# Performance work log

Measured on AMD Instinct MI355X. Metric: run time of the kernel, lower is better.

Reference implementation:

```python
import jax, jax.numpy as jnp
import numpy as np

B0, K, H, W = 8, 1, 512, 512
S, CS, NMS, M = 25, 51, 5, 2048
REG_W, COV_POW = 1.0, 0.5

def _gauss_kernel(n):
    x = jnp.linspace(-1.0, 1.0, n)
    g = jnp.exp(-x * x / 0.5)
    return g / g.sum()

def _conv1d2d(x, k1d, horizontal, pad_h, pad_w):
    # x: [B,1,H,W]; replicates torch F.conv2d with the given (possibly asymmetric) padding
    kern = k1d.reshape(1, 1, 1, -1) if horizontal else k1d.reshape(1, 1, -1, 1)
    return jax.lax.conv_general_dilated(x, kern, (1, 1), [(pad_h, pad_h), (pad_w, pad_w)],
                                        dimension_numbers=("NCHW", "OIHW", "NCHW"))

def bilinear_sample(img, pts):
    # img [B,C,H,W], pts [B,N,2] (x,y in [-1,1]); grid_sample bilinear, align_corners=False, zero padding
    Bb, C, Hh, Ww = img.shape
    x = (pts[..., 0] + 1.0) * 0.5 * Ww - 0.5
    y = (pts[..., 1] + 1.0) * 0.5 * Hh - 0.5
    x0 = jnp.floor(x); y0 = jnp.floor(y)
    wx = x - x0; wy = y - y0
    x0i = x0.astype(jnp.int32); y0i = y0.astype(jnp.int32)
    flat = img.reshape(Bb, C, Hh * Ww)
    def tap(yi, xi, w):
        ok = ((yi >= 0) & (yi < Hh) & (xi >= 0) & (xi < Ww)).astype(img.dtype)
        idx = jnp.clip(yi, 0, Hh - 1) * Ww + jnp.clip(xi, 0, Ww - 1)  # [B,N]
        v = jnp.take_along_axis(flat, idx[:, None, :], axis=2)        # [B,C,N]
        return v * (w * ok)[:, None, :]
    return (tap(y0i, x0i, (1 - wy) * (1 - wx)) + tap(y0i, x0i + 1, (1 - wy) * wx)
            + tap(y0i + 1, x0i, wy * (1 - wx)) + tap(y0i + 1, x0i + 1, wy * wx))

def compute_matchability(keypoint_p, has_depth, Bt):
    G = _gauss_kernel(S)
    # NOTE: faithful to original asymmetric padding bug: pad H while convolving along W, then pad W while convolving along H
    s = _conv1d2d(keypoint_p.reshape(Bt, 1, H, W), G, True, S // 2, 0)
    s = _conv1d2d(s, G, False, 0, S // 2)
    log_p_hat = jax.nn.log_softmax(jnp.log(s.reshape(Bt, H * W) + 1e-8), axis=-1)
    sd = _conv1d2d(has_depth.reshape(Bt, 1, H, W), G, True, 0, S // 2)
    sd = _conv1d2d(sd, G, False, S // 2, 0).reshape(Bt, H * W)
    p = sd / sd.sum(-1, keepdims=True)
    return jnp.sum(jnp.where(p > 0, p * (jnp.log(jnp.maximum(p, 1e-30)) - log_p_hat), 0.0), axis=-1)

def sample_keypoints(sm):
    # sm [B,H,W]; coverage-reweighted NMS + top-k (topk=True, subpixel=False)
    wcov = jnp.exp(-jnp.square(jnp.linspace(-2.0, 2.0, CS)))
    ld = _conv1d2d(((sm + 1e-6) * 1e4)[:, None], wcov, True, 0, CS // 2)
    ld = _conv1d2d(ld, wcov, False, CS // 2, 0)[:, 0]
    sm = sm * (ld + 1e-8) ** (-COV_POW)
    p = NMS // 2
    mx = jax.lax.reduce_window(sm, -jnp.inf, jax.lax.max, (1, NMS, NMS), (1, 1, 1),
                               [(0, 0), (p, p), (p, p)])
    sm = sm * (sm == mx)
    _, inds = jax.lax.top_k(sm.reshape(-1, H * W), M)
    xs = (jnp.arange(W) + 0.5) * 2.0 / W - 1.0
    ys = (jnp.arange(H) + 0.5) * 2.0 / H - 1.0
    grid = jnp.stack(jnp.meshgrid(xs, ys, indexing="xy"), axis=-1).reshape(H * W, 2)
    return jnp.take(grid, inds, axis=0)  # [B,M,2] normalized (x,y)

def masked_log_softmax(logits, mask):
    return jax.nn.log_softmax(jnp.where(mask, logits, -1e9), axis=-1)

def _reward(d):
    return jnp.exp(-100.0 * d)

def _forward(scoremap, gt_warp_A2B, gt_warp_B2A, valid_A2B, valid_B2A, has_depth):
    sg = jax.lax.stop_gradient
    lA = scoremap[:B0].reshape(B0, K, H * W)
    lB = scoremap[B0:].reshape(B0, K, H * W)
    logits = jnp.concatenate([lA, lB], 0)                                   # [2B,K,HW]
    kp_p = jax.nn.softmax(logits.reshape(2 * B0, K * H * W), -1).reshape(2 * B0, K, H * W).sum(1)
    match_loss = compute_matchability(kp_p, sg(has_depth), 2 * B0).mean()
    # sparse branch is under torch.set_grad_enabled(False)
    kpts_A = sample_keypoints(sg(kp_p[:B0]).reshape(B0, H, W))
    kpts_B = sample_keypoints(sg(kp_p[B0:]).reshape(B0, H, W))
    kpts_A2B = bilinear_sample(sg(gt_warp_A2B[..., 2:]).transpose(0, 3, 1, 2), kpts_A).transpose(0, 2, 1)
    kpts_B2A = bilinear_sample(sg(gt_warp_B2A[..., 2:]).transpose(0, 3, 1, 2), kpts_B).transpose(0, 2, 1)
    legit_A2B = bilinear_sample(sg(valid_A2B)[:, None], kpts_A)[:, 0] > 0   # [B,M]
    legit_B2A = bilinear_sample(sg(valid_B2A)[:, None], kpts_B)[:, 0] > 0
    dA = jnp.sqrt(jnp.sum(jnp.square(kpts_A2B[:, :, None] - kpts_B[:, None]), -1) + 1e-12).min(-1)
    dB = jnp.sqrt(jnp.sum(jnp.square(kpts_B2A[:, :, None] - kpts_A[:, None]), -1) + 1e-12).min(-1)
    rA = _reward(dA); rB = _reward(dB)
    slA = bilinear_sample(lA.reshape(B0, 1, H, W), kpts_A)[:, 0]            # [B,M]
    slB = bilinear_sample(lB.reshape(B0, 1, H, W), kpts_B)[:, 0]
    lpA = masked_log_softmax(slA, legit_A2B)
    lpB = masked_log_softmax(slB, legit_B2A)
    sparse = -jnp.sum(jnp.where(legit_A2B, rA * lpA, 0.0)) - jnp.sum(jnp.where(legit_B2A, rB * lpB, 0.0))
    return sparse + REG_W * match_loss

def setup_inputs() -> dict:
    key = jax.random.key(0)
    ks = jax.random.split(key, 6)
    scoremap = jax.random.normal(ks[0], (2 * B0, K, H, W), jnp.float32)
    gt_warp_A2B = jax.random.uniform(ks[1], (B0, H, W, 4), jnp.float32, -1.0, 1.0)
    gt_warp_B2A = jax.random.uniform(ks[2], (B0, H, W, 4), jnp.float32, -1.0, 1.0)
    valid_A2B = (jax.random.uniform(ks[3], (B0, H, W)) > 0.3).astype(jnp.float32)
    valid_B2A = (jax.random.uniform(ks[4], (B0, H, W)) > 0.3).astype(jnp.float32)
    has_depth = (jax.random.uniform(ks[5], (2 * B0, H, W)) > 0.3).astype(jnp.float32)
    return dict(scoremap=scoremap, gt_warp_A2B=gt_warp_A2B, gt_warp_B2A=gt_warp_B2A,
                valid_A2B=valid_A2B, valid_B2A=valid_B2A, has_depth=has_depth)

def reference(scoremap, gt_warp_A2B, gt_warp_B2A, valid_A2B, valid_B2A, has_depth):
    return _forward(scoremap, gt_warp_A2B, gt_warp_B2A, valid_A2B, valid_B2A, has_depth)
```

## Files before the change

### kernel.cpp

```cpp
#include <hip/hip_runtime.h>

#define HH 512
#define WW 512
#define HW_ 262144
#define NIMG 16
#define MK 2048
#define CAPB 4096
#define SCAP 32768
#define SBUFN 768

static constexpr size_t OFF_B1    = 16777216;
static constexpr size_t OFF_SMALL = 50331648;
static constexpr size_t OFF_PP   = 4849664;
static constexpr size_t OFF_WXp  = 5111808;
static constexpr size_t OFF_WYp  = 5242880;
static constexpr size_t OFF_LG   = 5373952;
static constexpr size_t OFF_SL   = 5505024;
static constexpr size_t OFF_PMIN = 5636096;
static constexpr size_t OFF_HIST = 33554432;
static constexpr size_t OFF_SURV = 33554432 + 4194304;

#define CSTRIDE 32

__device__ __forceinline__ float wred64(float v) {
  for (int m = 1; m < 64; m <<= 1) v += __shfl_xor(v, m);
  return v;
}

__device__ __forceinline__ float coh_loadf(const float* p) {
  return __hip_atomic_load(p, __ATOMIC_RELAXED, __HIP_MEMORY_SCOPE_AGENT);
}

__device__ __forceinline__ void g25_wave0(float* g) {
  int t = threadIdx.x;
  if (t < 64) {
    float raw = 0.0f;
    if (t < 25) {
      float x = -1.0f + (float)t * (2.0f / 24.0f);
      raw = expf(-(x * x) / 0.5f);
    }
    float s = raw;
    for (int m = 1; m < 64; m <<= 1) s += __shfl_xor(s, m);
    if (t < 25) g[t] = raw / s;
  }
}
__device__ __forceinline__ void w51_wave0(float* wc) {
  int t = threadIdx.x;
  if (t < 51) {
    float x = -2.0f + (float)t * (4.0f / 50.0f);
    wc[t] = expf(-x * x);
  }
}

__global__ void __launch_bounds__(256)
k_pre(const float* __restrict__ x, const float* __restrict__ hd, float* A,
      float* sume, float* sumS, float* Zb) {
  __shared__ float g[25];
  __shared__ float gp[26];
  __shared__ float red[12];
  int tid = threadIdx.x;
  g25_wave0(g);
  if (tid == 0) {
    float c = 0.0f;
    gp[0] = 0.0f;
    for (int k = 0; k < 25; k++) { c += g[k]; gp[k + 1] = c; }
  }
  size_t base = (size_t)blockIdx.x * 1024;
  size_t e = base + tid * 4;
  float4 xs = *(const float4*)(x + e);
  float4 hs = *(const float4*)(hd + e);
  __syncthreads();
  int rem = (int)(e & (HW_ - 1));
  int y = rem >> 9, x0 = rem & 511;
  float wv;
  {
    int k0 = y - 499; if (k0 < 0) k0 = 0;
    int k1 = y + 12;  if (k1 > 24) k1 = 24;
    wv = gp[k1 + 1] - gp[k0];
  }
  float cwv[4], cpv[4];
#pragma unroll
  for (int q = 0; q < 4; q++) {
    int i = x0 + q;
    int lo = i - 487; if (lo < 0) lo = 0;
    int hi = i;       if (hi > 24) hi = 24;
    cwv[q] = gp[hi + 1] - gp[lo];
    int lo2 = i - 499; if (lo2 < 0) lo2 = 0;
    int hi2 = i + 12;  if (hi2 > 24) hi2 = 24;
    cpv[q] = gp[hi2 + 1] - gp[lo2];
  }
  float e0 = expf(xs.x), e1 = expf(xs.y), e2 = expf(xs.z), e3 = expf(xs.w);
  *(float4*)(A + e) = make_float4(e0, e1, e2, e3);
  float r0 = (e0 + e1) + (e2 + e3);
  float r1 = (e0 * cwv[0] + e1 * cwv[1] + e2 * cwv[2] + e3 * cwv[3]) * wv;
  float r2 = (hs.x * cpv[0] + hs.y * cpv[1] + hs.z * cpv[2] + hs.w * cpv[3]) * wv;
  r0 = wred64(r0); r1 = wred64(r1); r2 = wred64(r2);
  int wid = tid >> 6;
  if ((tid & 63) == 0) { red[wid] = r0; red[4 + wid] = r1; red[8 + wid] = r2; }
  __syncthreads();
  if (tid == 0) {
    int img = (int)(base >> 18);
    atomicAdd(&sume[img * CSTRIDE], red[0] + red[1] + red[2] + red[3]);
    atomicAdd(&sumS[img * CSTRIDE], red[4] + red[5] + red[6] + red[7]);
    atomicAdd(&Zb[img * CSTRIDE], red[8] + red[9] + red[10] + red[11]);
  }
}

__global__ void __launch_bounds__(256)
k_hconv(const float* __restrict__ A, const float* __restrict__ hd,
        const float* __restrict__ sume, float* b12) {
  __shared__ __align__(16) float ta[512];
  __shared__ __align__(16) float th[536];
  __shared__ float g[25];
  int tid = threadIdx.x;
  int blk = blockIdx.x;
  int img = blk >> 9;
  size_t rowoff = (size_t)blk * 512;
  g25_wave0(g);
  ((float2*)ta)[tid] = *(const float2*)(A + rowoff + tid * 2);
  ((float2*)(th + 12))[tid] = *(const float2*)(hd + rowoff + tid * 2);
  if (tid < 12) { th[tid] = 0.0f; th[524 + tid] = 0.0f; }
  __syncthreads();
  float inv = 1.0f / sume[img * CSTRIDE];
  int j = 2 * tid;
  float v1a = 0.0f, v1b = 0.0f;
  if (tid >= 6 && tid <= 249) {
    float w[26];
#pragma unroll
    for (int d = 0; d < 26; d++) w[d] = ta[j - 12 + d];
#pragma unroll
    for (int d = 0; d < 25; d++) {
      v1a = fmaf(g[d], w[d], v1a);
      v1b = fmaf(g[d], w[d + 1], v1b);
    }
  }
  float v2a = 0.0f, v2b = 0.0f;
  {
    float u[26];
#pragma unroll
    for (int d = 0; d < 26; d++) u[d] = th[j + d];
#pragma unroll
    for (int d = 0; d < 25; d++) {
      v2a = fmaf(g[d], u[d], v2a);
      v2b = fmaf(g[d], u[d + 1], v2b);
    }
  }
  *(float4*)(b12 + (rowoff + j) * 2) =
      make_float4(v1a * inv, v2a, v1b * inv, v2b);
}

__global__ void __launch_bounds__(256)
k_match(const float* __restrict__ b12,
        const float* __restrict__ sume, const float* sumS, const float* Zb,
        float* macc) {
  __shared__ float g[40];
  __shared__ float red4[4];
  int tid = threadIdx.x;
  g25_wave0(g);
  if (tid >= 25 && tid < 40) g[tid] = 0.0f;
  int blk = blockIdx.x;
  int img = blk >> 6;
  int ty = (blk >> 3) & 7;
  int tx = blk & 7;
  int y0 = ty * 64, x0 = tx * 64;
  const float* base12 = b12 + (size_t)img * HW_ * 2;
  float Z = Zb[img * CSTRIDE];
  float invs = 1.0f / sume[img * CSTRIDE];
  float logS = logf(sumS[img * CSTRIDE] * invs + (float)HW_ * 1e-8f);
  __syncthreads();
  int seg = tid >> 6;
  int c = tid & 63;
  int r0 = seg * 16;
  const float* colp = base12 + (size_t)(x0 + c) * 2;
  float s[16], d[16], wreg[16];
#pragma unroll
  for (int jj = 0; jj < 16; jj++) { s[jj] = 0.f; d[jj] = 0.f; wreg[jj] = 0.f; }
  int ybase = y0 + r0 - 12;
#pragma unroll
  for (int i = 0; i < 40; i++) {
    int y = ybase + i;
    float vx = 0.0f, vy = 0.0f;
    if ((unsigned)y < 512u) {
      float2 v = *(const float2*)(colp + (size_t)y * 1024);
      vx = v.x; vy = v.y;
    }
#pragma unroll
    for (int jj = 15; jj >= 1; jj--) wreg[jj] = wreg[jj - 1];
    wreg[0] = g[i];
#pragma unroll
    for (int jj = 0; jj < 16; jj++) {
      s[jj] = fmaf(wreg[jj], vx, s[jj]);
      d[jj] = fmaf(wreg[jj], vy, d[jj]);
    }
  }
  float acc = 0.0f;
#pragma unroll
  for (int jj = 0; jj < 16; jj++) {
    float p = d[jj] / Z;
    if (p > 0.0f)
      acc += p * (logf(fmaxf(p, 1e-30f)) - (logf(s[jj] + 1e-8f) - logS));
  }
  acc = wred64(acc);
  if ((tid & 63) == 0) red4[tid >> 6] = acc;
  __syncthreads();
  if (tid == 0)
    atomicAdd(macc, red4[0] + red4[1] + red4[2] + red4[3]);
}

__global__ void __launch_bounds__(256)
k_h51(const float* __restrict__ A, const float* __restrict__ sume, float* out,
      unsigned* __restrict__ hist) {
  __shared__ float wc[51];
  __shared__ __align__(16) float ta[564];
  int tid = threadIdx.x;
  int blk = blockIdx.x;
  int img = blk >> 9;
  size_t rowoff = (size_t)blk * 512;
  w51_wave0(wc);
  if (tid < 32)
    ((uint4*)hist)[(size_t)blk * 32 + tid] = make_uint4(0u, 0u, 0u, 0u);
  float s1 = 1e4f / sume[img * CSTRIDE];
  for (int i = tid; i < 562; i += 256) {
    int j = i - 25;
    ta[i] = ((unsigned)j < 512u) ? fmaf(A[rowoff + j], s1, 1e-2f) : 0.0f;
  }
  __syncthreads();
  int j = 2 * tid;
  float w[52];
#pragma unroll
  for (int d = 0; d < 52; d++) w[d] = ta[j + d];
  float va = 0.0f, vb = 0.0f;
#pragma unroll
  for (int d = 0; d < 51; d++) {
    va = fmaf(wc[d], w[d], va);
    vb = fmaf(wc[d], w[d + 1], vb);
  }
  ((float2*)out)[blk * 256 + tid] = make_float2(va, vb);
}

__global__ void __launch_bounds__(512, 6)
k_smwnms(const float* __restrict__ A, const float* __restrict__ sume,
         const float* __restrict__ b1,
         unsigned long long* surv, unsigned* scnt, unsigned* hist) {
  __shared__ float wc[53];
  __shared__ __align__(16) float tb1[119 * 68];
  __shared__ __align__(16) float tsm[68 * 68];
  __shared__ unsigned lcnt;
  __shared__ unsigned gbase;
  float* hm = tb1;
  unsigned long long* sbuf = (unsigned long long*)(tb1 + 4352);
  int tid = threadIdx.x;
  w51_wave0(wc);
  if (tid == 51 || tid == 52) wc[tid] = 0.0f;
  if (tid == 0) lcnt = 0;
  int blk = blockIdx.x;
  int img = blk >> 6;
  int ty = (blk >> 3) & 7;
  int tx = blk & 7;
  int y0 = ty * 64, x0 = tx * 64;
  const float* base = b1 + (size_t)img * HW_;
  {
    float2 vreg[8];
    int laddr[8];
#pragma unroll
    for (int k = 0; k < 8; k++) {
      int i = tid + k * 512;
      bool ok = (i < 119 * 34);
      int r = i / 34, c2 = i - r * 34;
      int y = y0 + r - 27;
      int x = x0 + c2 * 2 - 2;
      float2 v = make_float2(0.0f, 0.0f);
      if (ok && (unsigned)y < 512u && (unsigned)x < 512u)
        v = *(const float2*)(base + (size_t)y * 512 + x);
      vreg[k] = v;
      laddr[k] = ok ? (r * 68 + c2 * 2) : -1;
    }
#pragma unroll
    for (int k = 0; k < 8; k++)
      if (laddr[k] >= 0) *(float2*)(tb1 + laddr[k]) = vreg[k];
  }
  __syncthreads();
  float inv = 1.0f / sume[img * CSTRIDE];
  const float* abase = A + (size_t)img * HW_;
  if (tid < 23 * 17) {
    int rg = tid / 17, cg = tid - rg * 17;
    int r0 = rg * 3, c0 = cg * 4;
    int nr = (r0 <= 65) ? 3 : 2;
    float2 apre[3][2];
#pragma unroll
    for (int jj = 0; jj < 3; jj++) {
      int y = y0 + r0 + jj - 2;
      int xb = x0 + c0 - 2;
      apre[jj][0] = make_float2(0.f, 0.f);
      apre[jj][1] = make_float2(0.f, 0.f);
      if ((unsigned)y < 512u) {
        const float* ar = abase + (size_t)y * 512;
        if ((unsigned)xb < 512u) apre[jj][0] = *(const float2*)(ar + xb);
        if ((unsigned)(xb + 2) < 512u) apre[jj][1] = *(const float2*)(ar + xb + 2);
      }
    }
    float a0x = 0.f, a0y = 0.f, a0z = 0.f, a0w = 0.f;
    float a1x = 0.f, a1y = 0.f, a1z = 0.f, a1w = 0.f;
    float a2x = 0.f, a2y = 0.f, a2z = 0.f, a2w = 0.f;
    float w1 = 0.f, w2 = 0.f;
    const float* tp = tb1 + r0 * 68 + c0;
#pragma unroll 4
    for (int i = 0; i < 53; i++) {
      float4 v = *(const float4*)(tp + i * 68);
      float w0 = wc[i];
      a0x = fmaf(w0, v.x, a0x); a0y = fmaf(w0, v.y, a0y);
      a0z = fmaf(w0, v.z, a0z); a0w = fmaf(w0, v.w, a0w);
      a1x = fmaf(w1, v.x, a1x); a1y = fmaf(w1, v.y, a1y);
      a1z = fmaf(w1, v.z, a1z); a1w = fmaf(w1, v.w, a1w);
      a2x = fmaf(w2, v.x, a2x); a2y = fmaf(w2, v.y, a2y);
      a2z = fmaf(w2, v.z, a2z); a2w = fmaf(w2, v.w, a2w);
      w2 = w1; w1 = w0;
    }
    auto storerow = [&](int jj, float ax, float ay, float az, float aw,
                        float2 p0, float2 p1) {
      int r = r0 + jj;
      int y = y0 + r - 2;
      int xb = x0 + c0 - 2;
      float4 res = make_float4(-3.4e38f, -3.4e38f, -3.4e38f, -3.4e38f);
      if ((unsigned)y < 512u) {
        if ((unsigned)xb < 512u) {
          res.x = (p0.x * inv) / sqrtf(ax + 1e-8f);
          res.y = (p0.y * inv) / sqrtf(ay + 1e-8f);
        }
        if ((unsigned)(xb + 2) < 512u) {
          res.z = (p1.x * inv) / sqrtf(az + 1e-8f);
          res.w = (p1.y * inv) / sqrtf(aw + 1e-8f);
        }
      }
      *(float4*)(tsm + r * 68 + c0) = res;
    };
    storerow(0, a0x, a0y, a0z, a0w, apre[0][0], apre[0][1]);
    storerow(1, a1x, a1y, a1z, a1w, apre[1][0], apre[1][1]);
    if (nr == 3) storerow(2, a2x, a2y, a2z, a2w, apre[2][0], apre[2][1]);
  }
  __syncthreads();
  for (int i = tid; i < 68 * 16; i += 512) {
    int r = i >> 4, cg = i & 15;
    const float* row = tsm + r * 68 + cg * 4;
    float4 v0 = *(const float4*)(row);
    float4 v1 = *(const float4*)(row + 4);
    float p01 = fmaxf(v0.x, v0.y), p12 = fmaxf(v0.y, v0.z);
    float p23 = fmaxf(v0.z, v0.w), p34 = fmaxf(v0.w, v1.x);
    float p45 = fmaxf(v1.x, v1.y), p56 = fmaxf(v1.y, v1.z);
    float m0 = fmaxf(fmaxf(p01, p23), v1.x);
    float m1 = fmaxf(fmaxf(p12, p34), v1.y);
    float m2 = fmaxf(fmaxf(p23, p45), v1.z);
    float m3 = fmaxf(fmaxf(p34, p56), v1.w);
    *(float4*)(hm + r * 64 + cg * 4) = make_float4(m0, m1, m2, m3);
  }
  __syncthreads();
  for (int k0 = 0; k0 < 2; k0++) {
    int i = tid + k0 * 512;
    int r = i >> 4, cb = (i & 15) * 4;
    const float* tp2 = tsm + (r + 2) * 68 + cb + 2;
    float2 va = *(const float2*)(tp2);
    float2 vb = *(const float2*)(tp2 + 2);
    float4 m0 = *(const float4*)(hm + r * 64 + cb);
    float4 m1 = *(const float4*)(hm + (r + 1) * 64 + cb);
    float4 m2 = *(const float4*)(hm + (r + 2) * 64 + cb);
    float4 m3 = *(const float4*)(hm + (r + 3) * 64 + cb);
    float4 m4 = *(const float4*)(hm + (r + 4) * 64 + cb);
    float Mx = fmaxf(fmaxf(m0.x, m1.x), fmaxf(fmaxf(m2.x, m3.x), m4.x));
    float My = fmaxf(fmaxf(m0.y, m1.y), fmaxf(fmaxf(m2.y, m3.y), m4.y));
    float Mz = fmaxf(fmaxf(m0.z, m1.z), fmaxf(fmaxf(m2.z, m3.z), m4.z));
    float Mw = fmaxf(fmaxf(m0.w, m1.w), fmaxf(fmaxf(m2.w, m3.w), m4.w));
    auto keepf = [&](float vk, float Mk, int k) {
      if (vk == Mk && vk != 0.0f) {
        unsigned p = atomicAdd(&lcnt, 1u);
        unsigned bits = __float_as_uint(vk);
        unsigned idx = (unsigned)((y0 + r) * 512 + x0 + cb + k);
        if (p < SBUFN)
          sbuf[p] = ((unsigned long long)bits << 32) |
                    (unsigned long long)(idx ^ 0xFFFFFFFFu);
        atomicAdd(&hist[(size_t)img * 65536 + (bits >> 16)], 1u);
      }
    };
    keepf(va.x, Mx, 0); keepf(va.y, My, 1);
    keepf(vb.x, Mz, 2); keepf(vb.y, Mw, 3);
  }
  __syncthreads();
  unsigned total = lcnt; if (total > SBUFN) total = SBUFN;
  if (tid == 0) gbase = atomicAdd(&scnt[img * CSTRIDE], total);
  __syncthreads();
  unsigned gb = gbase;
  for (unsigned i = tid; i < total; i += 512) {
    unsigned p = gb + i;
    if (p < SCAP) surv[(size_t)img * SCAP + p] = sbuf[i];
  }
}

__global__ void __launch_bounds__(1024)
k_select(const unsigned long long* __restrict__ surv,
         const unsigned* __restrict__ scnt,
         const unsigned* __restrict__ hist,
         const float* __restrict__ scoremap,
         const float* __restrict__ gtA, const float* __restrict__ gtB,
         const float* __restrict__ vA, const float* __restrict__ vB,
         float2* pp, float* wx, float* wy, float* lg, float* sl) {
  int img = blockIdx.x;
  __shared__ unsigned long long key[CAPB];
  __shared__ unsigned selbuf[MK];
  __shared__ unsigned wsum[16];
  __shared__ unsigned wpre[16];
  __shared__ unsigned cnts[2];
  __shared__ unsigned TbS, needS;
  int t = threadIdx.x;
  if (t < 2) cnts[t] = 0;
  const unsigned* h = hist + (size_t)img * 65536;
  int b0 = 65472 - 64 * t;
  const uint4* hv = (const uint4*)(h + b0);
  unsigned s = 0;
#pragma unroll
  for (int k = 0; k < 16; k++) {
    uint4 u = hv[k];
    s += u.x + u.y + u.z + u.w;
  }
  if (b0 == 0) s += 0x00100000u - h[0];
  unsigned inc = s;
  for (int m = 1; m < 64; m <<= 1) {
    unsigned o = __shfl_up(inc, m);
    if ((t & 63) >= m) inc += o;
  }
  if ((t & 63) == 63) wsum[t >> 6] = inc;
  __syncthreads();
  if (t < 16) {
    unsigned p = 0;
    for (int k = 0; k < 16; k++) if (k < t) p += wsum[k];
    wpre[t] = p;
  }
  __syncthreads();
  unsigned pre = wpre[t >> 6] + inc - s;
  if (pre < MK && pre + s >= MK) {
    unsigned c = pre;
    for (int k = 0; k < 64; k++) {
      int bin = 65535 - (t * 64 + k);
      unsigned cnt = (bin == 0) ? 0x00100000u : h[bin];
      if (c + cnt >= MK) { TbS = (unsigned)bin; needS = MK - c; break; }
      c += cnt;
    }
  }
  __syncthreads();
  unsigned T = TbS, need = needS;
  unsigned cnt = scnt[img * CSTRIDE]; if (cnt > SCAP) cnt = SCAP;
  const unsigned long long* sv = surv + (size_t)img * SCAP;
  for (unsigned i = t; i < SCAP; i += 1024) {
    if (i < cnt) {
      unsigned long long entry = sv[i];
      unsigned bin = (unsigned)(entry >> 48);
      if (bin > T) {
        unsigned p = atomicAdd(&cnts[0], 1u);
        if (p < MK) selbuf[p] = (unsigned)(entry & 0xFFFFFFFFull) ^ 0xFFFFFFFFu;
      } else if (bin == T) {
        unsigned p = atomicAdd(&cnts[1], 1u);
        if (p < CAPB) key[p] = entry;
      }
    }
  }
  __syncthreads();
  unsigned c1 = cnts[0]; if (c1 > MK) c1 = MK;
  unsigned bn = cnts[1];
  int n = (bn < CAPB) ? (int)bn : CAPB;
  int np2 = 2;
  while (np2 < n) np2 <<= 1;
  for (int k = t; k < np2; k += 1024)
    if (k >= n) key[k] = 0ull;
  __syncthreads();
  for (int sz = 2; sz <= np2; sz <<= 1) {
    for (int st = sz >> 1; st > 0; st >>= 1) {
      for (int i = t; i < np2; i += 1024) {
        int l = i ^ st;
        if (l > i) {
          unsigned long long a = key[i], b = key[l];
          bool up = ((i & sz) == 0);
          if (up ? (a < b) : (a > b)) { key[i] = b; key[l] = a; }
        }
      }
      __syncthreads();
    }
  }
  unsigned kk = need; if (kk > MK - c1) kk = MK - c1;
  for (unsigned m = t; m < MK - c1; m += 1024) {
    unsigned v = 0u;
    if (m < kk && m < (unsigned)n)
      v = (unsigned)(key[m] & 0xFFFFFFFFull) ^ 0xFFFFFFFFu;
    selbuf[c1 + m] = v;
  }
  __syncthreads();
  int b = (img < 8) ? img : img - 8;
  const float* gt = (img < 8) ? gtA : gtB;
  const float* vv = (img < 8) ? vA : vB;
  for (int q = t; q < MK; q += 1024) {
    int tt = img * MK + q;
    unsigned idx = selbuf[q] & (HW_ - 1);
    int hh = idx >> 9, wp = idx & 511;
    pp[tt] = make_float2((wp + 0.5f) * (2.0f / 512.0f) - 1.0f,
                         (hh + 0.5f) * (2.0f / 512.0f) - 1.0f);
    size_t pix = (size_t)b * HW_ + idx;
    float2 gxy = *(const float2*)(gt + pix * 4 + 2);
    wx[tt] = gxy.x;
    wy[tt] = gxy.y;
    lg[tt] = (vv[pix] > 0.0f) ? 1.0f : 0.0f;
    sl[tt] = scoremap[(size_t)img * HW_ + idx];
  }
}

__global__ void __launch_bounds__(256)
k_mindist(const float2* __restrict__ pp,
          const float* __restrict__ wx, const float* __restrict__ wy,
          float* pmin,
          const float* __restrict__ sl, const float* __restrict__ lg,
          float* sacc, float* macc, float* out,
          unsigned* mdone, unsigned* ldone) {
  __shared__ float2 opp[512];
  __shared__ unsigned rank_s;
  __shared__ float red[1024];
  int blk = blockIdx.x;
  int img = blk >> 5;
  int qc = (blk >> 2) & 7;
  int oc = blk & 3;
  const float2* ob = pp + (size_t)(img ^ 8) * MK + oc * 512;
  for (int k = threadIdx.x; k < 512; k += 256) opp[k] = ob[k];
  __syncthreads();
  int m = img * MK + qc * 256 + threadIdx.x;
  float ax = wx[m], ay = wy[m];
  float d[8];
#pragma unroll
  for (int u = 0; u < 8; u++) d[u] = 3.4e38f;
  for (int n = 0; n < 512; n += 8) {
#pragma unroll
    for (int u = 0; u < 8; u++) {
      float2 o = opp[n + u];
      float dx = ax - o.x, dy = ay - o.y;
      d[u] = fminf(d[u], fmaf(dx, dx, dy * dy));
    }
  }
  float d2 = fminf(fminf(fminf(d[0], d[1]), fminf(d[2], d[3])),
                   fminf(fminf(d[4], d[5]), fminf(d[6], d[7])));
  pmin[oc * (NIMG * MK) + m] = d2;
  __syncthreads();
  if (threadIdx.x == 0) {
    __threadfence();
    rank_s = atomicAdd(&mdone[img * CSTRIDE], 1u);
  }
  __syncthreads();
  if (rank_s != 31) return;
  __threadfence();
  int t = threadIdx.x;
  const int ST = NIMG * MK;
  float l0s[4], l1s[4], s0s[4], s1s[4], g0s[4], g1s[4];
#pragma unroll
  for (int u = 0; u < 4; u++) {
    int t0 = t + u * 256;
    int i0 = img * MK + t0, i1 = i0 + 1024;
    float s0 = sl[i0], s1 = sl[i1];
    float g0 = lg[i0], g1 = lg[i1];
    s0s[u] = s0; s1s[u] = s1; g0s[u] = g0; g1s[u] = g1;
    float l0 = (g0 > 0.0f) ? s0 : -1e9f;
    float l1 = (g1 > 0.0f) ? s1 : -1e9f;
    l0s[u] = l0; l1s[u] = l1;
    red[t0] = fmaxf(l0, l1);
  }
  __syncthreads();
  for (int sd = 512; sd > 0; sd >>= 1) {
    for (int k = t; k < sd; k += 256) red[k] = fmaxf(red[k], red[k + sd]);
    __syncthreads();
  }
  float mx = red[0];
  __syncthreads();
#pragma unroll
  for (int u = 0; u < 4; u++) {
    int t0 = t + u * 256;
    red[t0] = expf(l0s[u] - mx) + expf(l1s[u] - mx);
  }
  __syncthreads();
  for (int sd = 512; sd > 0; sd >>= 1) {
    for (int k = t; k < sd; k += 256) red[k] += red[k + sd];
    __syncthreads();
  }
  float lse = mx + logf(red[0]);
  __syncthreads();
#pragma unroll
  for (int u = 0; u < 4; u++) {
    int t0 = t + u * 256;
    int i0 = img * MK + t0, i1 = i0 + 1024;
    float a = 0.0f;
    if (g0s[u] > 0.0f) {
      float mn = fminf(fminf(coh_loadf(&pmin[i0]), coh_loadf(&pmin[ST + i0])),
                       fminf(coh_loadf(&pmin[2 * ST + i0]), coh_loadf(&pmin[3 * ST + i0])));
      float r0 = expf(-100.0f * sqrtf(mn + 1e-12f));
      a += r0 * (s0s[u] - lse);
    }
    if (g1s[u] > 0.0f) {
      float mn = fminf(fminf(coh_loadf(&pmin[i1]), coh_loadf(&pmin[ST + i1])),
                       fminf(coh_loadf(&pmin[2 * ST + i1]), coh_loadf(&pmin[3 * ST + i1])));
      float r1 = expf(-100.0f * sqrtf(mn + 1e-12f));
      a += r1 * (s1s[u] - lse);
    }
    red[t0] = a;
  }
  __syncthreads();
  for (int sd = 512; sd > 0; sd >>= 1) {
    for (int k = t; k < sd; k += 256) red[k] += red[k + sd];
    __syncthreads();
  }
  float tot = red[0];
  if (t == 0) {
    atomicAdd(sacc, -tot);
    __threadfence();
    unsigned dnum = atomicAdd(ldone, 1u);
    if (dnum == NIMG - 1) {
      float sv = atomicAdd(sacc, 0.0f);
      float mv = atomicAdd(macc, 0.0f);
      out[0] = sv + mv * (1.0f / 16.0f);
    }
  }
}

extern "C" void kernel_launch(void* const* d_in, const int* in_sizes, int n_in,
                              void* d_out, int out_size, void* d_ws, size_t ws_size,
                              hipStream_t stream) {
  const float* scoremap = (const float*)d_in[0];
  const float* gtA = (const float*)d_in[1];
  const float* gtB = (const float*)d_in[2];
  const float* vA  = (const float*)d_in[3];
  const float* vB  = (const float*)d_in[4];
  const float* hd  = (const float*)d_in[5];

  char* ws = (char*)d_ws;
  float* A   = (float*)(ws);
  float* B12 = (float*)(ws + OFF_B1);
  float* B1p = (float*)(ws + OFF_B1);

  char* sm = ws + OFF_SMALL;
  float*    sume   = (float*)(sm + 0);
  float*    sumS   = (float*)(sm + 2048);
  float*    Zb     = (float*)(sm + 4096);
  float*    macc   = (float*)(sm + 14336);
  float*    sacc   = (float*)(sm + 14464);
  unsigned* scnt   = (unsigned*)(sm + 16384);
  unsigned* ldone  = (unsigned*)(sm + 20480);
  unsigned* mdone  = (unsigned*)(sm + 24576);

  unsigned* hist = (unsigned*)(ws + OFF_HIST);
  unsigned long long* surv = (unsigned long long*)(ws + OFF_SURV);
  float2* pp = (float2*)(ws + OFF_PP);
  float* wx = (float*)(ws + OFF_WXp);
  float* wy = (float*)(ws + OFF_WYp);
  float* lg = (float*)(ws + OFF_LG);
  float* sl = (float*)(ws + OFF_SL);
  float* pmin = (float*)(ws + OFF_PMIN);

  float* out = (float*)d_out;

  hipMemsetAsync(sm, 0, 32768, stream);

  k_pre<<<4096, 256, 0, stream>>>(scoremap, hd, A, sume, sumS, Zb);

  k_hconv<<<8192, 256, 0, stream>>>(A, hd, sume, B12);
  k_match<<<1024, 256, 0, stream>>>(B12, sume, sumS, Zb, macc);

  k_h51<<<8192, 256, 0, stream>>>(A, sume, B1p, hist);

  k_smwnms<<<1024, 512, 0, stream>>>(A, sume, B1p, surv, scnt, hist);

  k_select<<<16, 1024, 0, stream>>>(surv, scnt, hist, scoremap, gtA, gtB,
                                    vA, vB, pp, wx, wy, lg, sl);

  k_mindist<<<512, 256, 0, stream>>>(pp, wx, wy, pmin, sl, lg,
                                     sacc, macc, out, mdone, ldone);
}
```

Measured before the change: 307.1 us.

## Split top-k selection into last-block threshold, parallel collect, and sort kernels

The histogram threshold search moves into the last finishing k_smwnms block for each image, found with an atomic done-counter. The survivor scan, previously done by 16 blocks of 1024 threads, becomes a separate 2048-block kernel that uses wave-ballot atomics to fill global selected and boundary buffers. The final kernel only sorts the boundary bin and gathers outputs. This spreads the serial per-image work across many more blocks, at the cost of an extra launch and extra global traffic.

```diff
diff --git a/kernel.cpp b/kernel.cpp
--- a/kernel.cpp
+++ b/kernel.cpp
@@ -11,6 +11,8 @@
 
 static constexpr size_t OFF_B1    = 16777216;
 static constexpr size_t OFF_SMALL = 50331648;
+static constexpr size_t OFF_SEL  = 4194304;
+static constexpr size_t OFF_BND  = 4325376;
 static constexpr size_t OFF_PP   = 4849664;
 static constexpr size_t OFF_WXp  = 5111808;
 static constexpr size_t OFF_WYp  = 5242880;
@@ -28,6 +30,9 @@
 }
 
 __device__ __forceinline__ float coh_loadf(const float* p) {
+  return __hip_atomic_load(p, __ATOMIC_RELAXED, __HIP_MEMORY_SCOPE_AGENT);
+}
+__device__ __forceinline__ unsigned coh_loadu(const unsigned* p) {
   return __hip_atomic_load(p, __ATOMIC_RELAXED, __HIP_MEMORY_SCOPE_AGENT);
 }
 
@@ -241,12 +246,16 @@
 __global__ void __launch_bounds__(512, 6)
 k_smwnms(const float* __restrict__ A, const float* __restrict__ sume,
          const float* __restrict__ b1,
-         unsigned long long* surv, unsigned* scnt, unsigned* hist) {
+         unsigned long long* surv, unsigned* scnt, unsigned* hist,
+         unsigned* Tb, unsigned* needb, unsigned* sdone) {
   __shared__ float wc[53];
   __shared__ __align__(16) float tb1[119 * 68];
   __shared__ __align__(16) float tsm[68 * 68];
   __shared__ unsigned lcnt;
   __shared__ unsigned gbase;
+  __shared__ unsigned rank_s;
+  __shared__ unsigned wsum8[8];
+  __shared__ unsigned wpre8[8];
   float* hm = tb1;
   unsigned long long* sbuf = (unsigned long long*)(tb1 + 4352);
   int tid = threadIdx.x;
@@ -392,83 +401,110 @@
     unsigned p = gb + i;
     if (p < SCAP) surv[(size_t)img * SCAP + p] = sbuf[i];
   }
+  __syncthreads();
+  if (tid == 0) {
+    __threadfence();
+    rank_s = atomicAdd(&sdone[img * CSTRIDE], 1u);
+  }
+  __syncthreads();
+  if (rank_s != 63) return;
+  {
+    const unsigned* h = hist + (size_t)img * 65536;
+    int t = tid;
+    int b0 = 65408 - 128 * t;
+    unsigned s = 0;
+    for (int k = 0; k < 128; k++) s += coh_loadu(h + b0 + k);
+    if (b0 == 0) s += 0x00100000u - coh_loadu(h);
+    unsigned inc = s;
+    for (int m = 1; m < 64; m <<= 1) {
+      unsigned o = __shfl_up(inc, m);
+      if ((t & 63) >= m) inc += o;
+    }
+    if ((t & 63) == 63) wsum8[t >> 6] = inc;
+    __syncthreads();
+    if (t < 8) {
+      unsigned p = 0;
+      for (int k = 0; k < 8; k++) if (k < t) p += wsum8[k];
+      wpre8[t] = p;
+    }
+    __syncthreads();
+    unsigned pre = wpre8[t >> 6] + inc - s;
+    if (pre < MK && pre + s >= MK) {
+      unsigned c = pre;
+      for (int k = 0; k < 128; k++) {
+        int bin = 65535 - (t * 128 + k);
+        unsigned cntb = (bin == 0) ? 0x00100000u : coh_loadu(h + bin);
+        if (c + cntb >= MK) {
+          Tb[img * CSTRIDE] = (unsigned)bin;
+          needb[img * CSTRIDE] = MK - c;
+          break;
+        }
+        c += cntb;
+      }
+    }
+  }
+}
+
+__global__ void k_collect(const unsigned long long* __restrict__ surv,
+                          const unsigned* __restrict__ scnt,
+                          const unsigned* __restrict__ Tb,
+                          unsigned* selcnt, unsigned* sel,
+                          unsigned* bcnt, unsigned long long* bnd) {
+  int blk = blockIdx.x;
+  int img = blk >> 7;
+  int i = (blk & 127) * 256 + threadIdx.x;
+  unsigned cnt = scnt[img * CSTRIDE]; if (cnt > SCAP) cnt = SCAP;
+  unsigned long long entry = ((unsigned)i < cnt) ? surv[(size_t)img * SCAP + i] : 0ull;
+  unsigned bits = (unsigned)(entry >> 32);
+  unsigned bin = bits >> 16;
+  unsigned T = Tb[img * CSTRIDE];
+  bool ok = (unsigned)i < cnt;
+  bool c1 = ok && (bin > T);
+  bool c2 = ok && (bin == T);
+  int lane = threadIdx.x & 63;
+  unsigned long long lowmask = (1ull << lane) - 1ull;
+
+  unsigned long long m1 = __ballot(c1);
+  if (m1) {
+    int leader = __ffsll(m1) - 1;
+    unsigned base = 0;
+    if (lane == leader) base = atomicAdd(&selcnt[img * CSTRIDE], (unsigned)__popcll(m1));
+    base = __shfl(base, leader);
+    if (c1) {
+      unsigned p = base + (unsigned)__popcll(m1 & lowmask);
+      if (p < MK) sel[img * MK + p] = (unsigned)(entry & 0xFFFFFFFFull) ^ 0xFFFFFFFFu;
+    }
+  }
+  unsigned long long m2 = __ballot(c2);
+  if (m2) {
+    int leader = __ffsll(m2) - 1;
+    unsigned base = 0;
+    if (lane == leader) base = atomicAdd(&bcnt[img * CSTRIDE], (unsigned)__popcll(m2));
+    base = __shfl(base, leader);
+    if (c2) {
+      unsigned p = base + (unsigned)__popcll(m2 & lowmask);
+      if (p < CAPB) bnd[(size_t)img * CAPB + p] = entry;
+    }
+  }
 }
 
 __global__ void __launch_bounds__(1024)
-k_select(const unsigned long long* __restrict__ surv,
-         const unsigned* __restrict__ scnt,
-         const unsigned* __restrict__ hist,
-         const float* __restrict__ scoremap,
-         const float* __restrict__ gtA, const float* __restrict__ gtB,
-         const float* __restrict__ vA, const float* __restrict__ vB,
-         float2* pp, float* wx, float* wy, float* lg, float* sl) {
+k_fsp(const unsigned long long* __restrict__ bnd, const unsigned* bcnt,
+      const unsigned* needb, const unsigned* selcnt,
+      const unsigned* __restrict__ sel,
+      const float* __restrict__ scoremap,
+      const float* __restrict__ gtA, const float* __restrict__ gtB,
+      const float* __restrict__ vA, const float* __restrict__ vB,
+      float2* pp, float* wx, float* wy, float* lg, float* sl) {
   int img = blockIdx.x;
   __shared__ unsigned long long key[CAPB];
-  __shared__ unsigned selbuf[MK];
-  __shared__ unsigned wsum[16];
-  __shared__ unsigned wpre[16];
-  __shared__ unsigned cnts[2];
-  __shared__ unsigned TbS, needS;
-  int t = threadIdx.x;
-  if (t < 2) cnts[t] = 0;
-  const unsigned* h = hist + (size_t)img * 65536;
-  int b0 = 65472 - 64 * t;
-  const uint4* hv = (const uint4*)(h + b0);
-  unsigned s = 0;
-#pragma unroll
-  for (int k = 0; k < 16; k++) {
-    uint4 u = hv[k];
-    s += u.x + u.y + u.z + u.w;
-  }
-  if (b0 == 0) s += 0x00100000u - h[0];
-  unsigned inc = s;
-  for (int m = 1; m < 64; m <<= 1) {
-    unsigned o = __shfl_up(inc, m);
-    if ((t & 63) >= m) inc += o;
-  }
-  if ((t & 63) == 63) wsum[t >> 6] = inc;
-  __syncthreads();
-  if (t < 16) {
-    unsigned p = 0;
-    for (int k = 0; k < 16; k++) if (k < t) p += wsum[k];
-    wpre[t] = p;
-  }
-  __syncthreads();
-  unsigned pre = wpre[t >> 6] + inc - s;
-  if (pre < MK && pre + s >= MK) {
-    unsigned c = pre;
-    for (int k = 0; k < 64; k++) {
-      int bin = 65535 - (t * 64 + k);
-      unsigned cnt = (bin == 0) ? 0x00100000u : h[bin];
-      if (c + cnt >= MK) { TbS = (unsigned)bin; needS = MK - c; break; }
-      c += cnt;
-    }
-  }
-  __syncthreads();
-  unsigned T = TbS, need = needS;
-  unsigned cnt = scnt[img * CSTRIDE]; if (cnt > SCAP) cnt = SCAP;
-  const unsigned long long* sv = surv + (size_t)img * SCAP;
-  for (unsigned i = t; i < SCAP; i += 1024) {
-    if (i < cnt) {
-      unsigned long long entry = sv[i];
-      unsigned bin = (unsigned)(entry >> 48);
-      if (bin > T) {
-        unsigned p = atomicAdd(&cnts[0], 1u);
-        if (p < MK) selbuf[p] = (unsigned)(entry & 0xFFFFFFFFull) ^ 0xFFFFFFFFu;
-      } else if (bin == T) {
-        unsigned p = atomicAdd(&cnts[1], 1u);
-        if (p < CAPB) key[p] = entry;
-      }
-    }
-  }
-  __syncthreads();
-  unsigned c1 = cnts[0]; if (c1 > MK) c1 = MK;
-  unsigned bn = cnts[1];
+  unsigned bn = bcnt[img * CSTRIDE];
   int n = (bn < CAPB) ? (int)bn : CAPB;
   int np2 = 2;
   while (np2 < n) np2 <<= 1;
+  int t = threadIdx.x;
   for (int k = t; k < np2; k += 1024)
-    if (k >= n) key[k] = 0ull;
+    key[k] = (k < n) ? bnd[(size_t)img * CAPB + k] : 0ull;
   __syncthreads();
   for (int sz = 2; sz <= np2; sz <<= 1) {
     for (int st = sz >> 1; st > 0; st >>= 1) {
@@ -483,20 +519,24 @@
       __syncthreads();
     }
   }
+  unsigned c1 = selcnt[img * CSTRIDE]; if (c1 > MK) c1 = MK;
+  unsigned need = needb[img * CSTRIDE];
   unsigned kk = need; if (kk > MK - c1) kk = MK - c1;
-  for (unsigned m = t; m < MK - c1; m += 1024) {
-    unsigned v = 0u;
-    if (m < kk && m < (unsigned)n)
-      v = (unsigned)(key[m] & 0xFFFFFFFFull) ^ 0xFFFFFFFFu;
-    selbuf[c1 + m] = v;
-  }
-  __syncthreads();
   int b = (img < 8) ? img : img - 8;
   const float* gt = (img < 8) ? gtA : gtB;
   const float* vv = (img < 8) ? vA : vB;
   for (int q = t; q < MK; q += 1024) {
+    unsigned v;
+    if ((unsigned)q < c1) {
+      v = sel[img * MK + q];
+    } else {
+      unsigned m = (unsigned)q - c1;
+      v = 0u;
+      if (m < kk && m < (unsigned)n)
+        v = (unsigned)(key[m] & 0xFFFFFFFFull) ^ 0xFFFFFFFFu;
+    }
     int tt = img * MK + q;
-    unsigned idx = selbuf[q] & (HW_ - 1);
+    unsigned idx = v & (HW_ - 1);
     int hh = idx >> 9, wp = idx & 511;
     pp[tt] = make_float2((wp + 0.5f) * (2.0f / 512.0f) - 1.0f,
                          (hh + 0.5f) * (2.0f / 512.0f) - 1.0f);
@@ -640,14 +680,21 @@
   float*    sume   = (float*)(sm + 0);
   float*    sumS   = (float*)(sm + 2048);
   float*    Zb     = (float*)(sm + 4096);
+  unsigned* Tb     = (unsigned*)(sm + 6144);
+  unsigned* needb  = (unsigned*)(sm + 8192);
+  unsigned* selcnt = (unsigned*)(sm + 10240);
+  unsigned* bcnt   = (unsigned*)(sm + 12288);
   float*    macc   = (float*)(sm + 14336);
   float*    sacc   = (float*)(sm + 14464);
   unsigned* scnt   = (unsigned*)(sm + 16384);
   unsigned* ldone  = (unsigned*)(sm + 20480);
   unsigned* mdone  = (unsigned*)(sm + 24576);
+  unsigned* sdone  = (unsigned*)(sm + 28672);
 
   unsigned* hist = (unsigned*)(ws + OFF_HIST);
   unsigned long long* surv = (unsigned long long*)(ws + OFF_SURV);
+  unsigned* sel  = (unsigned*)(ws + OFF_SEL);
+  unsigned long long* bnd = (unsigned long long*)(ws + OFF_BND);
   float2* pp = (float2*)(ws + OFF_PP);
   float* wx = (float*)(ws + OFF_WXp);
   float* wy = (float*)(ws + OFF_WYp);
@@ -666,10 +713,13 @@
 
   k_h51<<<8192, 256, 0, stream>>>(A, sume, B1p, hist);
 
-  k_smwnms<<<1024, 512, 0, stream>>>(A, sume, B1p, surv, scnt, hist);
-
-  k_select<<<16, 1024, 0, stream>>>(surv, scnt, hist, scoremap, gtA, gtB,
-                                    vA, vB, pp, wx, wy, lg, sl);
+  k_smwnms<<<1024, 512, 0, stream>>>(A, sume, B1p, surv, scnt, hist,
+                                     Tb, needb, sdone);
+
+  k_collect<<<2048, 256, 0, stream>>>(surv, scnt, Tb, selcnt, sel, bcnt, bnd);
+
+  k_fsp<<<16, 1024, 0, stream>>>(bnd, bcnt, needb, selcnt, sel, scoremap,
+                                 gtA, gtB, vA, vB, pp, wx, wy, lg, sl);
 
   k_mindist<<<512, 256, 0, stream>>>(pp, wx, wy, pmin, sl, lg,
                                      sacc, macc, out, mdone, ldone);
```

Result: slower. 433.9 us (+41.3%).
